# Kernel optimization log

Hardware: AMD Instinct MI355X
Metric: run time of the kernel (lower is better)

The kernel has to match this reference:

```python
import jax, jax.numpy as jnp
import numpy as np

DIM = 1024
NUM_HEADS = 16
DH = DIM // NUM_HEADS  # 64
B, S = 4, 2048


def setup_inputs() -> dict:
    key = jax.random.key(0)
    ks = jax.random.split(key, 9)
    sc = 0.02
    x = jax.random.normal(ks[0], (B, S, DIM), dtype=jnp.float32)
    # per-head projection weights stacked: [H, DIM, DH] (input-major layout)
    Wq = jax.random.normal(ks[1], (NUM_HEADS, DIM, DH), dtype=jnp.float32) * sc
    Wk = jax.random.normal(ks[2], (NUM_HEADS, DIM, DH), dtype=jnp.float32) * sc
    Wv = jax.random.normal(ks[3], (NUM_HEADS, DIM, DH), dtype=jnp.float32) * sc
    bq = jax.random.normal(ks[4], (NUM_HEADS, DH), dtype=jnp.float32) * sc
    bk = jax.random.normal(ks[5], (NUM_HEADS, DH), dtype=jnp.float32) * sc
    bv = jax.random.normal(ks[6], (NUM_HEADS, DH), dtype=jnp.float32) * sc
    Wo = jax.random.normal(ks[7], (DIM, DIM), dtype=jnp.float32) * sc  # (in, out)
    bo = jax.random.normal(ks[8], (DIM,), dtype=jnp.float32) * sc
    return {"x": x, "Wq": Wq, "Wk": Wk, "Wv": Wv,
            "bq": bq, "bk": bk, "bv": bv, "Wo": Wo, "bo": bo}


def reference(x, Wq, Wk, Wv, bq, bk, bv, Wo, bo):
    # Per-head Linear projections, vectorized over heads: [B,H,S,DH]
    q = jnp.einsum('bsd,hde->bhse', x, Wq) + bq[None, :, None, :]
    k = jnp.einsum('bsd,hde->bhse', x, Wk) + bk[None, :, None, :]
    v = jnp.einsum('bsd,hde->bhse', x, Wv) + bv[None, :, None, :]
    # attention_matmul: Q @ K^T normalized by sqrt(dim_per_head)
    scale = 1.0 / jnp.sqrt(jnp.asarray(DH, dtype=x.dtype))
    scores = jnp.einsum('bhse,bhte->bhst', q, k) * scale  # [B,H,S,S]
    attn = jax.nn.softmax(scores, axis=-1)
    # attn_drop with p=0.0 is identity
    o = jnp.einsum('bhst,bhte->bhse', attn, v)  # [B,H,S,DH]
    # concat along last dim in head order -> [B,S,H*DH]
    o = jnp.transpose(o, (0, 2, 1, 3)).reshape(x.shape[0], x.shape[1], NUM_HEADS * DH)
    # output projection (proj_drop p=0.0 is identity)
    return o @ Wo + bo
```

## Files before the change

### kernel.cpp

```cpp
#include <hip/hip_runtime.h>
#include <stdint.h>

#define DIM 1024
#define NH 16
#define DH 64
#define BATCH 4
#define SEQ 2048
#define MROWS (BATCH*SEQ)

typedef _Float16 half8 __attribute__((ext_vector_type(8)));
typedef __fp16 fp16x2 __attribute__((ext_vector_type(2)));
typedef float f32x4 __attribute__((ext_vector_type(4)));
typedef float f32x16 __attribute__((ext_vector_type(16)));
typedef unsigned int u32x2 __attribute__((ext_vector_type(2)));

__device__ __forceinline__ unsigned short f2h(float f) {
    union { _Float16 h; unsigned short u; } c; c.h = (_Float16)f; return c.u;
}
__device__ __forceinline__ unsigned int pk2u(float a, float b) {
    union { fp16x2 h; unsigned int u; } c;
    c.h = __builtin_amdgcn_cvt_pkrtz(a, b);
    return c.u;
}
__device__ __forceinline__ float fexp2(float x) {
    return __builtin_amdgcn_exp2f(x);
}
__device__ __forceinline__ void gl_lds16(const unsigned short* g, unsigned short* l) {
    __builtin_amdgcn_global_load_lds(
        (__attribute__((address_space(1))) void*)(void*)g,
        (__attribute__((address_space(3))) void*)(void*)l,
        16, 0, 0);
}

__global__ __launch_bounds__(256) void cast_prep_kernel(
    const float* __restrict__ x, unsigned short* __restrict__ xh,
    const float* __restrict__ Wq, const float* __restrict__ Wk,
    const float* __restrict__ Wv, const float* __restrict__ Wo,
    unsigned short* __restrict__ wt, unsigned short* __restrict__ wot)
{
    __shared__ unsigned short tile[64][65];
    const int bid = blockIdx.x;
    if (bid < 8192) {
        const int i = bid * 256 + threadIdx.x;
        float4 v = reinterpret_cast<const float4*>(x)[i];
        uint2 o;
        o.x = pk2u(v.x, v.y);
        o.y = pk2u(v.z, v.w);
        reinterpret_cast<uint2*>(xh)[i] = o;
        return;
    }
    const int local = bid - 8192;
    const int d0 = (local & 15) * 64;
    const int y = (local >> 4) & 15;
    const int mat = local >> 8;
    const int c = threadIdx.x & 63;
    const int rr = threadIdx.x >> 6;

    if (mat < 3) {
        const float* W = (mat == 0) ? Wq : ((mat == 1) ? Wk : Wv);
#pragma unroll
        for (int p = 0; p < 16; p++) {
            int dl = p * 4 + rr;
            tile[dl][c] = f2h(W[((size_t)y * 1024 + d0 + dl) * 64 + c]);
        }
        __syncthreads();
#pragma unroll
        for (int p = 0; p < 16; p++) {
            int el = p * 4 + rr;
            wt[(((size_t)(mat * NH + y) * 64) + el) * DIM + d0 + c] = tile[c][el];
        }
    } else {
        const int o0 = y * 64;
#pragma unroll
        for (int p = 0; p < 16; p++) {
            int dl = p * 4 + rr;
            tile[dl][c] = f2h(Wo[(size_t)(d0 + dl) * DIM + o0 + c]);
        }
        __syncthreads();
#pragma unroll
        for (int p = 0; p < 16; p++) {
            int ol = p * 4 + rr;
            wot[(size_t)(o0 + ol) * DIM + d0 + c] = tile[c][ol];
        }
    }
}

__global__ __launch_bounds__(256) void qkv_gemm_kernel(
    const unsigned short* __restrict__ xh,
    const unsigned short* __restrict__ wt,
    const float* __restrict__ bq, const float* __restrict__ bk,
    const float* __restrict__ bv,
    unsigned short* __restrict__ Qb,
    unsigned short* __restrict__ Kb,
    unsigned short* __restrict__ Vt)
{
    const int bid = blockIdx.x;
    const int xcd = bid & 7;
    const int local = bid >> 3;
    const int rowblk = xcd * 8 + local / 24;
    const int rem = local % 24;
    const int hpair = rem & 7;
    const int mat = rem >> 3;

    const int wave = threadIdx.x >> 6;
    const int lane = threadIdx.x & 63;
    const int ql = lane & 31;
    const int hi = lane >> 5;
    const int mhalf = wave & 1;
    const int nhalf = wave >> 1;

    __shared__ __align__(16) unsigned short pool[16384];
    unsigned short* AbP = pool;
    unsigned short* BtP = pool + 8192;

    const unsigned short* Asrc = xh + (size_t)rowblk * 128 * DIM;
    const unsigned short* Bsrc = wt + (size_t)(mat * NH + hpair * 2) * DH * DIM;

    const int srow = lane >> 2;
    const int scs = lane & 3;

    f32x16 z16;
#pragma unroll
    for (int e = 0; e < 16; e++) z16[e] = 0.f;
    f32x16 acc[2][2];
#pragma unroll
    for (int mt = 0; mt < 2; mt++)
#pragma unroll
        for (int nt = 0; nt < 2; nt++) acc[mt][nt] = z16;

    auto stage = [&](int k0, int sel) {
#pragma unroll
        for (int jj = 0; jj < 2; jj++) {
            const int j = wave * 2 + jj;
            const int r = j * 16 + srow;
            const int cg = scs ^ ((srow >> 1) & 3) ^ ((j * 2 + (srow >> 3)) & 3);
            gl_lds16(Asrc + (size_t)r * DIM + k0 + cg * 8, AbP + sel * 4096 + j * 512);
            gl_lds16(Bsrc + (size_t)r * DIM + k0 + cg * 8, BtP + sel * 4096 + j * 512);
        }
    };

    const int slotx = ((ql >> 1) & 3) ^ ((ql >> 3) & 3);
    int arow[2], brow[2], sks[2];
#pragma unroll
    for (int t = 0; t < 2; t++) {
        arow[t] = (mhalf * 64 + t * 32 + ql) * 32;
        brow[t] = (nhalf * 64 + t * 32 + ql) * 32;
    }
#pragma unroll
    for (int ks = 0; ks < 2; ks++) sks[ks] = ((ks * 2 + hi) ^ slotx) * 8;

    stage(0, 0);
    __syncthreads();

    for (int i = 0; i < DIM / 32; i++) {
        const int sel = i & 1;
        if (i + 1 < DIM / 32) stage((i + 1) * 32, sel ^ 1);

#pragma unroll
        for (int ks = 0; ks < 2; ks++) {
            half8 a0 = *reinterpret_cast<const half8*>(AbP + sel * 4096 + arow[0] + sks[ks]);
            half8 a1 = *reinterpret_cast<const half8*>(AbP + sel * 4096 + arow[1] + sks[ks]);
            half8 b0 = *reinterpret_cast<const half8*>(BtP + sel * 4096 + brow[0] + sks[ks]);
            half8 b1 = *reinterpret_cast<const half8*>(BtP + sel * 4096 + brow[1] + sks[ks]);
            acc[0][0] = __builtin_amdgcn_mfma_f32_32x32x16_f16(a0, b0, acc[0][0], 0, 0, 0);
            acc[0][1] = __builtin_amdgcn_mfma_f32_32x32x16_f16(a0, b1, acc[0][1], 0, 0, 0);
            acc[1][0] = __builtin_amdgcn_mfma_f32_32x32x16_f16(a1, b0, acc[1][0], 0, 0, 0);
            acc[1][1] = __builtin_amdgcn_mfma_f32_32x32x16_f16(a1, b1, acc[1][1], 0, 0, 0);
        }
        __syncthreads();
    }

    const float* bias = (mat == 0) ? bq : ((mat == 1) ? bk : bv);
    const float scale = (mat == 0) ? 0.1803368801111601f : 1.0f;
    const int rowBase = rowblk * 128 + mhalf * 64;
    const int bb = rowBase / SEQ;
    const int sBase = rowBase % SEQ;

    if (mat < 2) {
        unsigned short* outp = (mat == 0) ? Qb : Kb;
#pragma unroll
        for (int mt = 0; mt < 2; mt++) {
#pragma unroll
            for (int nt = 0; nt < 2; nt++) {
                const int e = nhalf * 64 + nt * 32 + ql;
                const int head = hpair * 2 + (e >> 6);
                const int n = e & 63;
                const float bvl = bias[head * DH + n];
                const size_t base = (size_t)(bb * NH + head) * SEQ * DH;
#pragma unroll
                for (int r = 0; r < 16; r++) {
                    const int s = sBase + mt * 32 + (r & 3) + 8 * (r >> 2) + 4 * hi;
                    outp[base + (size_t)s * DH + n] =
                        f2h((acc[mt][nt][r] + bvl) * scale);
                }
            }
        }
    } else {
#pragma unroll
        for (int mt = 0; mt < 2; mt++) {
#pragma unroll
            for (int nt = 0; nt < 2; nt++) {
                const int el = nhalf * 64 + nt * 32 + ql;
                const int head = hpair * 2 + (el >> 6);
                const int n = el & 63;
                const float bvl = bias[head * DH + n];
                const int xsw = (el & 7) << 2;
#pragma unroll
                for (int g = 0; g < 4; g++) {
                    const int slot = mhalf * 16 + mt * 8 + 2 * g + hi;
                    uint2 w;
                    w.x = pk2u(acc[mt][nt][4 * g + 0] + bvl, acc[mt][nt][4 * g + 1] + bvl);
                    w.y = pk2u(acc[mt][nt][4 * g + 2] + bvl, acc[mt][nt][4 * g + 3] + bvl);
                    *reinterpret_cast<uint2*>(pool + el * 128 + (slot ^ xsw) * 4) = w;
                }
            }
        }
        __syncthreads();
        const int blkRow = rowblk * 128;
        const int vb = blkRow / SEQ;
        const int s0b = blkRow % SEQ;
        const int sc = threadIdx.x & 15;
        const int esub = threadIdx.x >> 4;
#pragma unroll
        for (int p = 0; p < 8; p++) {
            const int el = p * 16 + esub;
            const int head = hpair * 2 + (el >> 6);
            const int n = el & 63;
            const int rs = (sc * 2) ^ ((el & 7) << 2);
            uint4 v = *reinterpret_cast<const uint4*>(pool + el * 128 + rs * 4);
            const size_t base = (size_t)(vb * NH + head) * DH * SEQ;
            *reinterpret_cast<uint4*>(&Vt[base + (size_t)n * SEQ + s0b + sc * 8]) = v;
        }
    }
}

__global__ __launch_bounds__(256, 4) void attn_kernel(
    const unsigned short* __restrict__ Qb,
    const unsigned short* __restrict__ Kb,
    const unsigned short* __restrict__ Vt,
    unsigned short* __restrict__ Ob)
{
    const int bid = blockIdx.x;
    const int xcd = bid & 7;
    const int local = bid >> 3;
    const int bhg = xcd * 8 + (local >> 4);
    const int qblk = local & 15;
    const int h = bhg & 15;
    const int bb = bhg >> 4;

    const int wave = threadIdx.x >> 6;
    const int lane = threadIdx.x & 63;
    const int ql = lane & 31;
    const int hi = lane >> 5;
    const int qBase = qblk * 128 + wave * 32;

    const size_t bh = (size_t)(bb * NH + h);
    const unsigned short* Qh = Qb + bh * SEQ * DH;
    const unsigned short* Kh = Kb + bh * SEQ * DH;
    const unsigned short* Vh = Vt + bh * DH * SEQ;

    __shared__ __align__(16) unsigned short Kbuf[2][64 * 64];
    __shared__ __align__(16) unsigned short Vbuf[2][64 * 64];

    const int srow = lane >> 3;
    const int scs = lane & 7;
    int koff[2], voff[2];
#pragma unroll
    for (int jj = 0; jj < 2; jj++) {
        const int r = wave * 16 + jj * 8 + srow;
        const int cg = scs ^ srow ^ ((wave * 2 + jj) & 3);
        koff[jj] = r * DH + cg * 8;
        voff[jj] = r * SEQ + cg * 8;
    }

    auto stage_k = [&](int kt, int sel) {
        const size_t base = (size_t)kt * 64 * DH;
        gl_lds16(Kh + base + koff[0], &Kbuf[sel][wave * 1024]);
        gl_lds16(Kh + base + koff[1], &Kbuf[sel][wave * 1024 + 512]);
    };
    auto stage_v = [&](int kt, int sel) {
        const size_t base = (size_t)kt * 64;
        gl_lds16(Vh + base + voff[0], &Vbuf[sel][wave * 1024]);
        gl_lds16(Vh + base + voff[1], &Vbuf[sel][wave * 1024 + 512]);
    };

    half8 qf[4];
#pragma unroll
    for (int ks = 0; ks < 4; ks++)
        qf[ks] = *reinterpret_cast<const half8*>(
            Qh + (size_t)(qBase + ql) * DH + ks * 16 + hi * 8);

    const int slotx = (ql & 7) ^ ((ql >> 3) & 3);
    int rowb[2], soff[4];
#pragma unroll
    for (int b = 0; b < 2; b++) rowb[b] = (b * 32 + ql) * 64;
#pragma unroll
    for (int ks = 0; ks < 4; ks++) soff[ks] = ((ks * 2 + hi) ^ slotx) * 8;

    f32x16 z16;
#pragma unroll
    for (int e = 0; e < 16; e++) z16[e] = 0.f;

    f32x16 o[2];
#pragma unroll
    for (int mt = 0; mt < 2; mt++) o[mt] = z16;
    float lsA = 0.f, lsB = 0.f;
    half8 pf[4];

    auto burst = [&](int sel, bool doPV) {
        f32x16 sacc[2];
        __builtin_amdgcn_s_setprio(1);
#pragma unroll
        for (int ks = 0; ks < 4; ks++) {
#pragma unroll
            for (int b = 0; b < 2; b++) {
                half8 kf = *reinterpret_cast<const half8*>(
                    &Kbuf[sel][rowb[b] + soff[ks]]);
                sacc[b] = __builtin_amdgcn_mfma_f32_32x32x16_f16(
                    kf, qf[ks], ks ? sacc[b] : z16, 0, 0, 0);
            }
            if (doPV) {
#pragma unroll
                for (int mt = 0; mt < 2; mt++) {
                    half8 vf = *reinterpret_cast<const half8*>(
                        &Vbuf[sel][rowb[mt] + soff[ks]]);
                    o[mt] = __builtin_amdgcn_mfma_f32_32x32x16_f16(
                        vf, pf[ks], o[mt], 0, 0, 0);
                }
            }
        }
        __builtin_amdgcn_s_setprio(0);

#pragma unroll
        for (int kb = 0; kb < 2; kb++) {
            unsigned int c[8];
#pragma unroll
            for (int m = 0; m < 8; m++) {
                float a = fexp2(sacc[kb][2 * m]);
                float b2 = fexp2(sacc[kb][2 * m + 1]);
                if (m & 1) lsB += a + b2; else lsA += a + b2;
                c[m] = pk2u(a, b2);
            }
#pragma unroll
            for (int ks = 0; ks < 2; ks++) {
                u32x2 w02 = __builtin_amdgcn_permlane32_swap(
                    c[4 * ks + 0], c[4 * ks + 2], false, false);
                u32x2 w13 = __builtin_amdgcn_permlane32_swap(
                    c[4 * ks + 1], c[4 * ks + 3], false, false);
                union { unsigned int u[4]; half8 h; } cv;
                cv.u[0] = w02[0]; cv.u[1] = w13[0];
                cv.u[2] = w02[1]; cv.u[3] = w13[1];
                pf[kb * 2 + ks] = cv.h;
            }
        }
    };

    stage_k(0, 0);
    __syncthreads();

    stage_k(1, 1);
    stage_v(0, 1);
    burst(0, false);
    __syncthreads();

    for (int i = 1; i < SEQ / 64; i++) {
        const int sel = i & 1;
        if (i + 1 < SEQ / 64) stage_k(i + 1, sel ^ 1);
        stage_v(i, sel ^ 1);
        burst(sel, true);
        __syncthreads();
    }

    __builtin_amdgcn_s_setprio(1);
#pragma unroll
    for (int ks = 0; ks < 4; ks++)
#pragma unroll
        for (int mt = 0; mt < 2; mt++) {
            half8 vf = *reinterpret_cast<const half8*>(
                &Vbuf[0][rowb[mt] + soff[ks]]);
            o[mt] = __builtin_amdgcn_mfma_f32_32x32x16_f16(
                vf, pf[ks], o[mt], 0, 0, 0);
        }
    __builtin_amdgcn_s_setprio(0);

    float l = lsA + lsB;
    l += __shfl_xor(l, 32);
    const float inv = 1.f / l;
    const size_t orow = (size_t)(bb * SEQ + qBase + ql) * DIM + h * DH;
#pragma unroll
    for (int mt = 0; mt < 2; mt++) {
#pragma unroll
        for (int g = 0; g < 4; g++) {
            uint2 pkd;
            pkd.x = pk2u(o[mt][4 * g + 0] * inv, o[mt][4 * g + 1] * inv);
            pkd.y = pk2u(o[mt][4 * g + 2] * inv, o[mt][4 * g + 3] * inv);
            *reinterpret_cast<uint2*>(Ob + orow + mt * 32 + 8 * g + 4 * hi) = pkd;
        }
    }
}

__global__ __launch_bounds__(256) void out_proj_kernel(
    const unsigned short* __restrict__ Ob,
    const unsigned short* __restrict__ wot,
    const float* __restrict__ bo,
    float* __restrict__ out)
{
    const int bid = blockIdx.x;
    const int xcd = bid & 7;
    const int local = bid >> 3;
    const int rowblk = xcd * 8 + (local >> 3);
    const int colblk = local & 7;

    const int wave = threadIdx.x >> 6;
    const int lane = threadIdx.x & 63;
    const int ql = lane & 31;
    const int hi = lane >> 5;
    const int mhalf = wave & 1;
    const int nhalf = wave >> 1;

    __shared__ __align__(16) unsigned short Ab[2][128 * 32];
    __shared__ __align__(16) unsigned short Bt[2][128 * 32];

    const unsigned short* Asrc = Ob + (size_t)rowblk * 128 * DIM;
    const unsigned short* Bsrc = wot + (size_t)colblk * 128 * DIM;

    const int srow = lane >> 2;
    const int scs = lane & 3;

    f32x16 z16;
#pragma unroll
    for (int e = 0; e < 16; e++) z16[e] = 0.f;
    f32x16 acc[2][2];
#pragma unroll
    for (int mt = 0; mt < 2; mt++)
#pragma unroll
        for (int nt = 0; nt < 2; nt++) acc[mt][nt] = z16;

    auto stage = [&](int k0, int sel) {
#pragma unroll
        for (int jj = 0; jj < 2; jj++) {
            const int j = wave * 2 + jj;
            const int r = j * 16 + srow;
            const int cg = scs ^ ((srow >> 1) & 3) ^ ((j * 2 + (srow >> 3)) & 3);
            gl_lds16(Asrc + (size_t)r * DIM + k0 + cg * 8, &Ab[sel][j * 512]);
            gl_lds16(Bsrc + (size_t)r * DIM + k0 + cg * 8, &Bt[sel][j * 512]);
        }
    };

    const int slotx = ((ql >> 1) & 3) ^ ((ql >> 3) & 3);
    int arow[2], brow[2], sks[2];
#pragma unroll
    for (int t = 0; t < 2; t++) {
        arow[t] = (mhalf * 64 + t * 32 + ql) * 32;
        brow[t] = (nhalf * 64 + t * 32 + ql) * 32;
    }
#pragma unroll
    for (int ks = 0; ks < 2; ks++) sks[ks] = ((ks * 2 + hi) ^ slotx) * 8;

    stage(0, 0);
    __syncthreads();

    for (int i = 0; i < DIM / 32; i++) {
        const int sel = i & 1;
        if (i + 1 < DIM / 32) stage((i + 1) * 32, sel ^ 1);

#pragma unroll
        for (int ks = 0; ks < 2; ks++) {
            half8 a0 = *reinterpret_cast<const half8*>(&Ab[sel][arow[0] + sks[ks]]);
            half8 a1 = *reinterpret_cast<const half8*>(&Ab[sel][arow[1] + sks[ks]]);
            half8 b0 = *reinterpret_cast<const half8*>(&Bt[sel][brow[0] + sks[ks]]);
            half8 b1 = *reinterpret_cast<const half8*>(&Bt[sel][brow[1] + sks[ks]]);
            acc[0][0] = __builtin_amdgcn_mfma_f32_32x32x16_f16(a0, b0, acc[0][0], 0, 0, 0);
            acc[0][1] = __builtin_amdgcn_mfma_f32_32x32x16_f16(a0, b1, acc[0][1], 0, 0, 0);
            acc[1][0] = __builtin_amdgcn_mfma_f32_32x32x16_f16(a1, b0, acc[1][0], 0, 0, 0);
            acc[1][1] = __builtin_amdgcn_mfma_f32_32x32x16_f16(a1, b1, acc[1][1], 0, 0, 0);
        }
        __syncthreads();
    }

    const int rowBase = rowblk * 128 + mhalf * 64;
    const int colBase = colblk * 128 + nhalf * 64;
#pragma unroll
    for (int mt = 0; mt < 2; mt++) {
#pragma unroll
        for (int nt = 0; nt < 2; nt++) {
            const int col = colBase + nt * 32 + ql;
            const float bias = bo[col];
#pragma unroll
            for (int r = 0; r < 16; r++) {
                const int row = rowBase + mt * 32 + (r & 3) + 8 * (r >> 2) + 4 * hi;
                out[(size_t)row * DIM + col] = acc[mt][nt][r] + bias;
            }
        }
    }
}


extern "C" void kernel_launch(void* const* d_in, const int* in_sizes, int n_in,
                              void* d_out, int out_size, void* d_ws, size_t ws_size,
                              hipStream_t stream) {
    const float* x  = (const float*)d_in[0];
    const float* Wq = (const float*)d_in[1];
    const float* Wk = (const float*)d_in[2];
    const float* Wv = (const float*)d_in[3];
    const float* bq = (const float*)d_in[4];
    const float* bk = (const float*)d_in[5];
    const float* bv = (const float*)d_in[6];
    const float* Wo = (const float*)d_in[7];
    const float* bo = (const float*)d_in[8];
    float* out = (float*)d_out;

    unsigned short* xh  = (unsigned short*)d_ws;
    unsigned short* wt  = xh  + (size_t)MROWS * DIM;
    unsigned short* wot = wt  + (size_t)3 * NH * DH * DIM;
    unsigned short* Qb  = wot + (size_t)DIM * DIM;
    unsigned short* Kb  = Qb  + (size_t)BATCH * NH * SEQ * DH;
    unsigned short* Vt  = Kb  + (size_t)BATCH * NH * SEQ * DH;
    unsigned short* Ob  = Vt  + (size_t)BATCH * NH * SEQ * DH;

    cast_prep_kernel<<<9216, 256, 0, stream>>>(x, xh, Wq, Wk, Wv, Wo, wt, wot);
    qkv_gemm_kernel<<<1536, 256, 0, stream>>>(xh, wt, bq, bk, bv, Qb, Kb, Vt);
    attn_kernel<<<1024, 256, 0, stream>>>(Qb, Kb, Vt, Ob);
    out_proj_kernel<<<512, 256, 0, stream>>>(Ob, wot, bo, out);
}
```

Measured before the change: 293.2 us.

## Replace software-pipelined QK/PV burst with per-block sequential compute loop

Removes the software pipeline that overlapped the next tile's QK^T MFMAs with the previous tile's PV MFMAs. Each 32-key sub-block now computes scores, runs exp, and immediately feeds P into the PV MFMAs for the same tile, with K and V staged together one tile ahead. This simplifies the prologue and epilogue and drops the four cross-iteration P fragments, lowering register pressure. In exchange, the exp/permlane work can no longer hide behind independent MFMAs and becomes a serial dependency.

```diff
diff --git a/kernel.cpp b/kernel.cpp
--- a/kernel.cpp
+++ b/kernel.cpp
@@ -305,42 +305,31 @@
 #pragma unroll
     for (int mt = 0; mt < 2; mt++) o[mt] = z16;
     float lsA = 0.f, lsB = 0.f;
-    half8 pf[4];
-
-    auto burst = [&](int sel, bool doPV) {
-        f32x16 sacc[2];
-        __builtin_amdgcn_s_setprio(1);
-#pragma unroll
-        for (int ks = 0; ks < 4; ks++) {
-#pragma unroll
-            for (int b = 0; b < 2; b++) {
+
+    auto compute = [&](int sel) {
+#pragma unroll
+        for (int kb = 0; kb < 2; kb++) {
+            f32x16 sacc;
+            __builtin_amdgcn_s_setprio(1);
+#pragma unroll
+            for (int ks = 0; ks < 4; ks++) {
                 half8 kf = *reinterpret_cast<const half8*>(
-                    &Kbuf[sel][rowb[b] + soff[ks]]);
-                sacc[b] = __builtin_amdgcn_mfma_f32_32x32x16_f16(
-                    kf, qf[ks], ks ? sacc[b] : z16, 0, 0, 0);
+                    &Kbuf[sel][rowb[kb] + soff[ks]]);
+                sacc = __builtin_amdgcn_mfma_f32_32x32x16_f16(
+                    kf, qf[ks], ks ? sacc : z16, 0, 0, 0);
             }
-            if (doPV) {
-#pragma unroll
-                for (int mt = 0; mt < 2; mt++) {
-                    half8 vf = *reinterpret_cast<const half8*>(
-                        &Vbuf[sel][rowb[mt] + soff[ks]]);
-                    o[mt] = __builtin_amdgcn_mfma_f32_32x32x16_f16(
-                        vf, pf[ks], o[mt], 0, 0, 0);
-                }
-            }
-        }
-        __builtin_amdgcn_s_setprio(0);
-
-#pragma unroll
-        for (int kb = 0; kb < 2; kb++) {
+            __builtin_amdgcn_s_setprio(0);
+
             unsigned int c[8];
 #pragma unroll
             for (int m = 0; m < 8; m++) {
-                float a = fexp2(sacc[kb][2 * m]);
-                float b2 = fexp2(sacc[kb][2 * m + 1]);
+                float a = fexp2(sacc[2 * m]);
+                float b2 = fexp2(sacc[2 * m + 1]);
                 if (m & 1) lsB += a + b2; else lsA += a + b2;
                 c[m] = pk2u(a, b2);
             }
+
+            __builtin_amdgcn_s_setprio(1);
 #pragma unroll
             for (int ks = 0; ks < 2; ks++) {
                 u32x2 w02 = __builtin_amdgcn_permlane32_swap(
@@ -350,38 +339,32 @@
                 union { unsigned int u[4]; half8 h; } cv;
                 cv.u[0] = w02[0]; cv.u[1] = w13[0];
                 cv.u[2] = w02[1]; cv.u[3] = w13[1];
-                pf[kb * 2 + ks] = cv.h;
+                const half8 pf = cv.h;
+#pragma unroll
+                for (int mt = 0; mt < 2; mt++) {
+                    half8 vf = *reinterpret_cast<const half8*>(
+                        &Vbuf[sel][rowb[mt] + soff[kb * 2 + ks]]);
+                    o[mt] = __builtin_amdgcn_mfma_f32_32x32x16_f16(
+                        vf, pf, o[mt], 0, 0, 0);
+                }
             }
+            __builtin_amdgcn_s_setprio(0);
         }
     };
 
     stage_k(0, 0);
+    stage_v(0, 0);
     __syncthreads();
 
-    stage_k(1, 1);
-    stage_v(0, 1);
-    burst(0, false);
-    __syncthreads();
-
-    for (int i = 1; i < SEQ / 64; i++) {
+    for (int i = 0; i < SEQ / 64; i++) {
         const int sel = i & 1;
-        if (i + 1 < SEQ / 64) stage_k(i + 1, sel ^ 1);
-        stage_v(i, sel ^ 1);
-        burst(sel, true);
+        if (i + 1 < SEQ / 64) {
+            stage_k(i + 1, sel ^ 1);
+            stage_v(i + 1, sel ^ 1);
+        }
+        compute(sel);
         __syncthreads();
     }
-
-    __builtin_amdgcn_s_setprio(1);
-#pragma unroll
-    for (int ks = 0; ks < 4; ks++)
-#pragma unroll
-        for (int mt = 0; mt < 2; mt++) {
-            half8 vf = *reinterpret_cast<const half8*>(
-                &Vbuf[0][rowb[mt] + soff[ks]]);
-            o[mt] = __builtin_amdgcn_mfma_f32_32x32x16_f16(
-                vf, pf[ks], o[mt], 0, 0, 0);
-        }
-    __builtin_amdgcn_s_setprio(0);
 
     float l = lsA + lsB;
     l += __shfl_xor(l, 32);
```

After: 284.2 us (median of 2 runs). -3.1%, faster.
